# Kernel tuning notes

Hardware: AMD Instinct MI355X
Metric: run time of the kernel (lower is better)

## Reference

```python
import jax, jax.numpy as jnp
import numpy as np

BATCH = 256
B_TYPES = 32   # input capsule types
C_TYPES = 10   # output capsule types
H, W = 8, 8    # input spatial extent == kernel (output is 1x1)
POSE = 16      # capsule pose length (shape (16,1))
NUM_ITER = 3
EPS = 1e-8


def setup_inputs() -> dict:
    key = jax.random.key(0)
    k1, k2, k3 = jax.random.split(key, 3)
    input_caps_poses = jax.random.normal(k1, (BATCH, B_TYPES, H, W, POSE, 1), jnp.float32)
    input_caps_activations = jax.random.uniform(k2, (BATCH, B_TYPES, H, W), jnp.float32)
    # nn.init.normal_(std=0.1) on [B, kh, kw, C, os0, is0]
    weight = 0.1 * jax.random.normal(k3, (B_TYPES, H, W, C_TYPES, POSE, POSE), jnp.float32)
    # routing_bias initialized to 0.1: [C, oh, ow, os0, os1]
    routing_bias = jnp.full((C_TYPES, 1, 1, POSE, 1), 0.1, jnp.float32)
    return {
        "input_caps_poses": input_caps_poses,
        "input_caps_activations": input_caps_activations,
        "weight": weight,
        "routing_bias": routing_bias,
    }


def _squash(s):
    # Hinton squash: ||s||^2/(1+||s||^2) * s/||s||, norm over pose dims
    n2 = jnp.sum(s * s, axis=(-2, -1), keepdims=True)
    return (n2 / (1.0 + n2)) * s * jax.lax.rsqrt(n2 + EPS)


def reference(input_caps_poses, input_caps_activations, weight, routing_bias):
    b = input_caps_poses.shape[0]
    # votes[b,c,B,h,w,o,p] = sum_i W[B,h,w,c,o,i] * pose[b,B,h,w,i,p]
    votes = jnp.einsum('Bhwcoi,bBhwip->bcBhwop', weight, input_caps_poses)
    logits = jnp.zeros((b, C_TYPES, B_TYPES, H, W), votes.dtype)
    bias = routing_bias.reshape(1, C_TYPES, POSE, 1)
    v = None
    for it in range(NUM_ITER):
        # coupling coefficients: softmax over output capsule types
        c = jax.nn.softmax(logits, axis=1)                      # [b,C,B,h,w]
        # weighted sum of votes over all input capsules (B,h,w)
        s = jnp.einsum('bcBhw,bcBhwop->bcop', c, votes) + bias  # [b,C,16,1]
        v = _squash(s)
        if it < NUM_ITER - 1:
            # agreement: dot(vote, output pose)
            logits = logits + jnp.einsum('bcBhwop,bcop->bcBhw', votes, v)
    output_caps_poses = v[:, :, None, None, :, :]               # [b,C,1,1,16,1]
    output_caps_activations = jnp.sqrt(
        jnp.sum(v * v, axis=(-2, -1)) + EPS)[:, :, None, None]  # [b,C,1,1]
    return output_caps_poses, output_caps_activations
```

## Files before the change

kernel.cpp:

```cpp
#include <hip/hip_runtime.h>
#include <hip/hip_fp16.h>
#include <math.h>


typedef _Float16 f16;
typedef _Float16 f16x2 __attribute__((ext_vector_type(2)));
typedef _Float16 f16x4 __attribute__((ext_vector_type(4)));
typedef __fp16   h16x2 __attribute__((ext_vector_type(2)));
typedef float f32x4 __attribute__((ext_vector_type(4)));

__device__ __forceinline__ f16x2 pk(float a, float b) {
    h16x2 t = __builtin_amdgcn_cvt_pkrtz(a, b);
    return __builtin_bit_cast(f16x2, t);
}

#if __has_builtin(__builtin_amdgcn_fdot2)
__device__ __forceinline__ float FDOT2(f16x2 a, f16x2 b, float c) {
    return __builtin_amdgcn_fdot2(__builtin_bit_cast(h16x2, a),
                                  __builtin_bit_cast(h16x2, b), c, false);
}
#else
__device__ __forceinline__ float FDOT2(f16x2 a, f16x2 b, float c) {
    return c + (float)a[0] * (float)b[0] + (float)a[1] * (float)b[1];
}
#endif

constexpr int XS_ROW = 76;

__device__ __forceinline__ float xorsum4(float v) {
    v += __shfl_xor(v, 16, 64);
    v += __shfl_xor(v, 32, 64);
    return v;
}

__device__ __forceinline__ f16x2 xorsum4h(f16x2 v) {
    union { f16x2 h; int i; } u;
    union { int i; f16x2 h; } w;
    u.h = v; w.i = __shfl_xor(u.i, 16, 64); v = v + w.h;
    u.h = v; w.i = __shfl_xor(u.i, 32, 64); v = v + w.h;
    return v;
}

__device__ __forceinline__ f16x4 cvt4(float4 w) {
    f16x2 a = pk(w.x, w.y);
    f16x2 b = pk(w.z, w.w);
    f16x4 r; r[0] = a[0]; r[1] = a[1]; r[2] = b[0]; r[3] = b[1];
    return r;
}

template<int PASS>
__global__ __launch_bounds__(256, 2)
void pass_k(const float* __restrict__ poses, const float* __restrict__ weight,
            const float* __restrict__ bias,
            const float* __restrict__ sp0, const float* __restrict__ sp1,
            float* __restrict__ s_dst)
{
    __shared__ f16 Ws[640 * 16];
    __shared__ f16 xs[64 * XS_ROW];

    const int tid  = threadIdx.x;
    const int blk  = blockIdx.x;
    const int ngrp = blk >> 2;
    const int b0   = (blk & 3) * 64;
    const int wave = tid >> 6;
    const int lane = tid & 63;
    const int q    = lane >> 4;
    const int lo   = lane & 15;
    const int wtb  = wave * 16;
    const int bg   = b0 + wtb;

    const int sr  = ((lo >> 1) ^ (lo >> 3)) & 3;
    const int xqE = ((q ^ sr) & 3) * 4;
    const int xqO = ((q ^ sr ^ 2) & 3) * 4;

    f16x2 vsp[10][2];
    if (PASS >= 1) {
        const int rowb = (bg + lo) * 10;
        #pragma unroll
        for (int c = 0; c < 10; ++c) {
            float4 bb = *(const float4*)(bias + c * 16 + q * 4);
            const size_t off = (size_t)(rowb + c) * 16 + q * 4;
            float4 sa = *(const float4*)(sp0 + off);
            float t0 = sa.x + bb.x, t1 = sa.y + bb.y;
            float t2 = sa.z + bb.z, t3 = sa.w + bb.w;
            float n2 = xorsum4(t0*t0 + t1*t1 + t2*t2 + t3*t3);
            float sc = n2 / (1.f + n2) * rsqrtf(n2 + 1e-8f);
            float v0 = sc*t0, v1 = sc*t1, v2 = sc*t2, v3 = sc*t3;
            if (PASS == 2) {
                float4 ua = *(const float4*)(sp1 + off);
                float u0 = ua.x + bb.x, u1 = ua.y + bb.y;
                float u2 = ua.z + bb.z, u3 = ua.w + bb.w;
                float m2 = xorsum4(u0*u0 + u1*u1 + u2*u2 + u3*u3);
                float sc2 = m2 / (1.f + m2) * rsqrtf(m2 + 1e-8f);
                v0 += sc2*u0; v1 += sc2*u1; v2 += sc2*u2; v3 += sc2*u3;
            }
            vsp[c][0] = pk(v0, v1);
            vsp[c][1] = pk(v2, v3);
        }
    }

    f16x4 wregh[10];
    f16x4 xregh[4];
    const int b_loc = tid >> 2, part = tid & 3;
    const int wcol = (((tid & 3) ^ ((tid >> 3) ^ (tid >> 5))) & 3) * 4;

    auto load_iter = [&](int l) {
        const float* wp = weight + (size_t)(ngrp * 2 + l) * 10240;
        #pragma unroll
        for (int k = 0; k < 10; ++k) {
            float4 t = ((const float4*)wp)[tid + k * 256];
            wregh[k] = cvt4(t);
        }
        const float* xp = poses + (size_t)(b0 + b_loc) * 32768
                          + (size_t)(ngrp * 8 + l * 4 + part) * 16;
        #pragma unroll
        for (int j = 0; j < 4; ++j) {
            float4 t = ((const float4*)xp)[j];
            xregh[j] = cvt4(t);
        }
    };
    auto store_iter = [&]() {
        #pragma unroll
        for (int k = 0; k < 10; ++k) {
            const int f = tid + k * 256;
            *(f16x4*)&Ws[(f >> 2) * 16 + wcol] = wregh[k];
        }
        f16* lp = xs + b_loc * XS_ROW + part * 16;
        #pragma unroll
        for (int j = 0; j < 4; ++j) *(f16x4*)&lp[j * 4] = xregh[j];
    };

    f32x4 acc[10];
    #pragma unroll
    for (int c = 0; c < 10; ++c) acc[c] = (f32x4){0.f, 0.f, 0.f, 0.f};

    load_iter(0);

    for (int l = 0; l < 2; ++l) {
        __syncthreads();
        store_iter();
        if (l + 1 < 2) load_iter(l + 1);
        __syncthreads();

        #pragma unroll
        for (int n = 0; n < 4; ++n) {
            f16x4 bx = *(const f16x4*)&xs[(wtb + lo) * XS_ROW + n * 16 + q * 4];
            f16x2 Vh[10][2];
            #pragma unroll
            for (int c = 0; c < 10; ++c) {
                f16x4 aw = *(const f16x4*)&Ws[((n * 10 + c) * 16 + lo) * 16
                                              + ((c & 1) ? xqO : xqE)];
                f32x4 V = __builtin_amdgcn_mfma_f32_16x16x16f16(
                    aw, bx, (f32x4){0.f, 0.f, 0.f, 0.f}, 0, 0, 0);
                Vh[c][0] = pk(V[0], V[1]);
                Vh[c][1] = pk(V[2], V[3]);
            }

            float cfv[10];
            if (PASS >= 1) {
                float lg[10];
                #pragma unroll
                for (int cp = 0; cp < 5; ++cp) {
                    const int c0 = cp * 2, c1 = cp * 2 + 1;
                    float p0 = FDOT2(Vh[c0][0], vsp[c0][0], 0.f);
                    p0 = FDOT2(Vh[c0][1], vsp[c0][1], p0);
                    float p1 = FDOT2(Vh[c1][0], vsp[c1][0], 0.f);
                    p1 = FDOT2(Vh[c1][1], vsp[c1][1], p1);
                    f16x2 pr = xorsum4h(pk(p0, p1));
                    lg[c0] = (float)pr[0];
                    lg[c1] = (float)pr[1];
                }
                float m = lg[0];
                #pragma unroll
                for (int c = 1; c < 10; ++c) m = fmaxf(m, lg[c]);
                float sum = 0.f;
                #pragma unroll
                for (int c = 0; c < 10; ++c) { lg[c] = __expf(lg[c] - m); sum += lg[c]; }
                const float inv = 1.f / sum;
                #pragma unroll
                for (int c = 0; c < 10; ++c) cfv[c] = lg[c] * inv;
            }

            #pragma unroll
            for (int c = 0; c < 10; ++c) {
                const float w = (PASS == 0) ? 1.f : cfv[c];
                acc[c][0] = fmaf(w, (float)Vh[c][0][0], acc[c][0]);
                acc[c][1] = fmaf(w, (float)Vh[c][0][1], acc[c][1]);
                acc[c][2] = fmaf(w, (float)Vh[c][1][0], acc[c][2]);
                acc[c][3] = fmaf(w, (float)Vh[c][1][1], acc[c][3]);
            }
        }
    }

    __syncthreads();
    float* tr = (float*)Ws + wave * 320;
    const float fs = (PASS == 0) ? 0.1f : 1.f;
    #pragma unroll
    for (int c = 0; c < 10; ++c) {
        *(float4*)&tr[lo * 20 + q * 4] = (float4){acc[c][0], acc[c][1], acc[c][2], acc[c][3]};
        float r0 = tr[(q * 4 + 0) * 20 + lo];
        float r1 = tr[(q * 4 + 1) * 20 + lo];
        float r2 = tr[(q * 4 + 2) * 20 + lo];
        float r3 = tr[(q * 4 + 3) * 20 + lo];
        float* sp = s_dst + ((size_t)(bg + q * 4) * 10 + c) * 16 + lo;
        unsafeAtomicAdd(sp + 0 * 160, fs * r0);
        unsafeAtomicAdd(sp + 1 * 160, fs * r1);
        unsafeAtomicAdd(sp + 2 * 160, fs * r2);
        unsafeAtomicAdd(sp + 3 * 160, fs * r3);
    }
}

__global__ __launch_bounds__(256)
void epi_k(const float* __restrict__ s2, const float* __restrict__ bias,
           float* __restrict__ out)
{
    const int t = blockIdx.x * 256 + threadIdx.x;
    if (t >= 2560) return;
    const int c = t % 10;
    const float* sp = s2 + (size_t)t * 16;
    const float* bp = bias + c * 16;
    float sv[16];
    float n2 = 0.f;
    #pragma unroll
    for (int o = 0; o < 16; ++o) { float v = sp[o] + bp[o]; sv[o] = v; n2 += v * v; }
    const float scale = n2 / (1.f + n2) * rsqrtf(n2 + 1e-8f);
    float a2 = 0.f;
    #pragma unroll
    for (int o = 0; o < 16; ++o) {
        float v = scale * sv[o];
        out[(size_t)t * 16 + o] = v;
        a2 += v * v;
    }
    out[40960 + t] = sqrtf(a2 + 1e-8f);
}

extern "C" void kernel_launch(void* const* d_in, const int* in_sizes, int n_in,
                              void* d_out, int out_size, void* d_ws, size_t ws_size,
                              hipStream_t stream)
{
    const float* poses  = (const float*)d_in[0];
    const float* weight = (const float*)d_in[2];
    const float* bias   = (const float*)d_in[3];
    float* out = (float*)d_out;
    float* s0 = (float*)d_ws;
    float* s1 = s0 + 40960;
    float* s2 = s1 + 40960;

    (void)hipMemsetAsync(d_ws, 0, 3 * 40960 * sizeof(float), stream);

    pass_k<0><<<1024, 256, 0, stream>>>(poses, weight, bias, nullptr, nullptr, s0);
    pass_k<1><<<1024, 256, 0, stream>>>(poses, weight, bias, s0, nullptr, s1);
    pass_k<2><<<1024, 256, 0, stream>>>(poses, weight, bias, s0, s1, s2);
    epi_k<<<10, 256, 0, stream>>>(s2, bias, out);
}
```

Measured before the change: 247.5 us.

## Fuse routing passes into one cooperative persistent kernel with LDS-resident data

Replaces the three per-iteration routing kernels and the epilogue with a single cooperative kernel of 256 blocks × 512 threads. Each block loads its weight slice and pose tile into LDS once as fp16, then runs all three routing passes with grid.sync between them. This avoids re-reading poses and weights from global memory on every pass and removes the extra launches. The cost is a larger LDS footprint per block and fewer resident blocks, plus grid-wide barriers. The fallback to a normal launch if the cooperative launch fails would deadlock or race at grid.sync.

```diff
diff --git a/kernel.cpp b/kernel.cpp
--- a/kernel.cpp
+++ b/kernel.cpp
@@ -1,6 +1,9 @@
 #include <hip/hip_runtime.h>
 #include <hip/hip_fp16.h>
+#include <hip/hip_cooperative_groups.h>
 #include <math.h>
+
+namespace cg = cooperative_groups;
 
 
 typedef _Float16 f16;
@@ -25,7 +28,7 @@
 }
 #endif
 
-constexpr int XS_ROW = 76;
+constexpr int XS_ROW = 268;
 
 __device__ __forceinline__ float xorsum4(float v) {
     v += __shfl_xor(v, 16, 64);
@@ -48,103 +51,102 @@
     return r;
 }
 
-template<int PASS>
-__global__ __launch_bounds__(256, 2)
-void pass_k(const float* __restrict__ poses, const float* __restrict__ weight,
-            const float* __restrict__ bias,
-            const float* __restrict__ sp0, const float* __restrict__ sp1,
-            float* __restrict__ s_dst)
+__global__ __launch_bounds__(512, 2)
+void fused_k(const float* __restrict__ poses, const float* __restrict__ weight,
+             const float* __restrict__ bias,
+             float* __restrict__ s0, float* __restrict__ s1,
+             float* __restrict__ s2, float* __restrict__ out)
 {
-    __shared__ f16 Ws[640 * 16];
-    __shared__ f16 xs[64 * XS_ROW];
+    __shared__ f16   Ws[2560 * 16];
+    __shared__ f16   xs[128 * XS_ROW];
+    __shared__ float tr[8 * 320];
 
     const int tid  = threadIdx.x;
     const int blk  = blockIdx.x;
-    const int ngrp = blk >> 2;
-    const int b0   = (blk & 3) * 64;
+    const int ngrp = blk >> 1;
+    const int b0   = (blk & 1) * 128;
     const int wave = tid >> 6;
     const int lane = tid & 63;
     const int q    = lane >> 4;
     const int lo   = lane & 15;
-    const int wtb  = wave * 16;
-    const int bg   = b0 + wtb;
+    const int bg   = b0 + wave * 16;
 
     const int sr  = ((lo >> 1) ^ (lo >> 3)) & 3;
     const int xqE = ((q ^ sr) & 3) * 4;
     const int xqO = ((q ^ sr ^ 2) & 3) * 4;
 
-    f16x2 vsp[10][2];
-    if (PASS >= 1) {
-        const int rowb = (bg + lo) * 10;
-        #pragma unroll
-        for (int c = 0; c < 10; ++c) {
-            float4 bb = *(const float4*)(bias + c * 16 + q * 4);
-            const size_t off = (size_t)(rowb + c) * 16 + q * 4;
-            float4 sa = *(const float4*)(sp0 + off);
-            float t0 = sa.x + bb.x, t1 = sa.y + bb.y;
-            float t2 = sa.z + bb.z, t3 = sa.w + bb.w;
-            float n2 = xorsum4(t0*t0 + t1*t1 + t2*t2 + t3*t3);
-            float sc = n2 / (1.f + n2) * rsqrtf(n2 + 1e-8f);
-            float v0 = sc*t0, v1 = sc*t1, v2 = sc*t2, v3 = sc*t3;
-            if (PASS == 2) {
-                float4 ua = *(const float4*)(sp1 + off);
-                float u0 = ua.x + bb.x, u1 = ua.y + bb.y;
-                float u2 = ua.z + bb.z, u3 = ua.w + bb.w;
-                float m2 = xorsum4(u0*u0 + u1*u1 + u2*u2 + u3*u3);
-                float sc2 = m2 / (1.f + m2) * rsqrtf(m2 + 1e-8f);
-                v0 += sc2*u0; v1 += sc2*u1; v2 += sc2*u2; v3 += sc2*u3;
-            }
-            vsp[c][0] = pk(v0, v1);
-            vsp[c][1] = pk(v2, v3);
-        }
-    }
-
-    f16x4 wregh[10];
-    f16x4 xregh[4];
-    const int b_loc = tid >> 2, part = tid & 3;
-    const int wcol = (((tid & 3) ^ ((tid >> 3) ^ (tid >> 5))) & 3) * 4;
-
-    auto load_iter = [&](int l) {
-        const float* wp = weight + (size_t)(ngrp * 2 + l) * 10240;
-        #pragma unroll
-        for (int k = 0; k < 10; ++k) {
-            float4 t = ((const float4*)wp)[tid + k * 256];
-            wregh[k] = cvt4(t);
-        }
+    {
+        const float* wp = weight + (size_t)ngrp * 40960;
+        const int wcol = (((tid & 3) ^ ((tid >> 3) ^ (tid >> 5))) & 3) * 4;
+        float4 wreg[10];
+        #pragma unroll
+        for (int half = 0; half < 2; ++half) {
+            #pragma unroll
+            for (int k = 0; k < 10; ++k)
+                wreg[k] = ((const float4*)wp)[tid + (half * 10 + k) * 512];
+            #pragma unroll
+            for (int k = 0; k < 10; ++k) {
+                const int f = tid + (half * 10 + k) * 512;
+                *(f16x4*)&Ws[(f >> 2) * 16 + wcol] = cvt4(wreg[k]);
+            }
+        }
+        const int b_loc = tid >> 2, part = tid & 3;
         const float* xp = poses + (size_t)(b0 + b_loc) * 32768
-                          + (size_t)(ngrp * 8 + l * 4 + part) * 16;
-        #pragma unroll
-        for (int j = 0; j < 4; ++j) {
-            float4 t = ((const float4*)xp)[j];
-            xregh[j] = cvt4(t);
-        }
-    };
-    auto store_iter = [&]() {
-        #pragma unroll
-        for (int k = 0; k < 10; ++k) {
-            const int f = tid + k * 256;
-            *(f16x4*)&Ws[(f >> 2) * 16 + wcol] = wregh[k];
-        }
-        f16* lp = xs + b_loc * XS_ROW + part * 16;
-        #pragma unroll
-        for (int j = 0; j < 4; ++j) *(f16x4*)&lp[j * 4] = xregh[j];
-    };
-
-    f32x4 acc[10];
-    #pragma unroll
-    for (int c = 0; c < 10; ++c) acc[c] = (f32x4){0.f, 0.f, 0.f, 0.f};
-
-    load_iter(0);
-
-    for (int l = 0; l < 2; ++l) {
-        __syncthreads();
-        store_iter();
-        if (l + 1 < 2) load_iter(l + 1);
-        __syncthreads();
-
-        #pragma unroll
-        for (int n = 0; n < 4; ++n) {
-            f16x4 bx = *(const f16x4*)&xs[(wtb + lo) * XS_ROW + n * 16 + q * 4];
+                          + (size_t)ngrp * 256 + part * 64;
+        float4 xreg[8];
+        #pragma unroll
+        for (int half = 0; half < 2; ++half) {
+            #pragma unroll
+            for (int j = 0; j < 8; ++j)
+                xreg[j] = ((const float4*)xp)[half * 8 + j];
+            #pragma unroll
+            for (int j = 0; j < 8; ++j)
+                *(f16x4*)&xs[b_loc * XS_ROW + part * 64 + (half * 8 + j) * 4]
+                    = cvt4(xreg[j]);
+        }
+    }
+    __syncthreads();
+
+    cg::grid_group grid = cg::this_grid();
+
+    #pragma unroll 1
+    for (int pass = 0; pass < 3; ++pass) {
+        float* dst = (pass == 0) ? s0 : (pass == 1) ? s1 : s2;
+        const float fs = (pass == 0) ? 0.1f : 1.f;
+
+        f16x2 vsp[10][2];
+        if (pass >= 1) {
+            const int rowb = (bg + lo) * 10;
+            #pragma unroll
+            for (int c = 0; c < 10; ++c) {
+                float4 bb = *(const float4*)(bias + c * 16 + q * 4);
+                const size_t off = (size_t)(rowb + c) * 16 + q * 4;
+                float4 sa = *(const float4*)(s0 + off);
+                float t0 = sa.x + bb.x, t1 = sa.y + bb.y;
+                float t2 = sa.z + bb.z, t3 = sa.w + bb.w;
+                float n2 = xorsum4(t0*t0 + t1*t1 + t2*t2 + t3*t3);
+                float sc = n2 / (1.f + n2) * rsqrtf(n2 + 1e-8f);
+                float v0 = sc*t0, v1 = sc*t1, v2 = sc*t2, v3 = sc*t3;
+                if (pass == 2) {
+                    float4 ua = *(const float4*)(s1 + off);
+                    float u0 = ua.x + bb.x, u1 = ua.y + bb.y;
+                    float u2 = ua.z + bb.z, u3 = ua.w + bb.w;
+                    float m2 = xorsum4(u0*u0 + u1*u1 + u2*u2 + u3*u3);
+                    float sc2 = m2 / (1.f + m2) * rsqrtf(m2 + 1e-8f);
+                    v0 += sc2*u0; v1 += sc2*u1; v2 += sc2*u2; v3 += sc2*u3;
+                }
+                vsp[c][0] = pk(v0, v1);
+                vsp[c][1] = pk(v2, v3);
+            }
+        }
+
+        f32x4 acc[10];
+        #pragma unroll
+        for (int c = 0; c < 10; ++c) acc[c] = (f32x4){0.f, 0.f, 0.f, 0.f};
+
+        #pragma unroll 2
+        for (int n = 0; n < 16; ++n) {
+            f16x4 bx = *(const f16x4*)&xs[(wave * 16 + lo) * XS_ROW + n * 16 + q * 4];
             f16x2 Vh[10][2];
             #pragma unroll
             for (int c = 0; c < 10; ++c) {
@@ -157,7 +159,9 @@
             }
 
             float cfv[10];
-            if (PASS >= 1) {
+            #pragma unroll
+            for (int c = 0; c < 10; ++c) cfv[c] = 1.f;
+            if (pass >= 1) {
                 float lg[10];
                 #pragma unroll
                 for (int cp = 0; cp < 5; ++cp) {
@@ -183,55 +187,52 @@
 
             #pragma unroll
             for (int c = 0; c < 10; ++c) {
-                const float w = (PASS == 0) ? 1.f : cfv[c];
-                acc[c][0] = fmaf(w, (float)Vh[c][0][0], acc[c][0]);
-                acc[c][1] = fmaf(w, (float)Vh[c][0][1], acc[c][1]);
-                acc[c][2] = fmaf(w, (float)Vh[c][1][0], acc[c][2]);
-                acc[c][3] = fmaf(w, (float)Vh[c][1][1], acc[c][3]);
-            }
-        }
-    }
-
-    __syncthreads();
-    float* tr = (float*)Ws + wave * 320;
-    const float fs = (PASS == 0) ? 0.1f : 1.f;
-    #pragma unroll
-    for (int c = 0; c < 10; ++c) {
-        *(float4*)&tr[lo * 20 + q * 4] = (float4){acc[c][0], acc[c][1], acc[c][2], acc[c][3]};
-        float r0 = tr[(q * 4 + 0) * 20 + lo];
-        float r1 = tr[(q * 4 + 1) * 20 + lo];
-        float r2 = tr[(q * 4 + 2) * 20 + lo];
-        float r3 = tr[(q * 4 + 3) * 20 + lo];
-        float* sp = s_dst + ((size_t)(bg + q * 4) * 10 + c) * 16 + lo;
-        unsafeAtomicAdd(sp + 0 * 160, fs * r0);
-        unsafeAtomicAdd(sp + 1 * 160, fs * r1);
-        unsafeAtomicAdd(sp + 2 * 160, fs * r2);
-        unsafeAtomicAdd(sp + 3 * 160, fs * r3);
-    }
-}
-
-__global__ __launch_bounds__(256)
-void epi_k(const float* __restrict__ s2, const float* __restrict__ bias,
-           float* __restrict__ out)
-{
-    const int t = blockIdx.x * 256 + threadIdx.x;
-    if (t >= 2560) return;
-    const int c = t % 10;
-    const float* sp = s2 + (size_t)t * 16;
-    const float* bp = bias + c * 16;
-    float sv[16];
-    float n2 = 0.f;
-    #pragma unroll
-    for (int o = 0; o < 16; ++o) { float v = sp[o] + bp[o]; sv[o] = v; n2 += v * v; }
-    const float scale = n2 / (1.f + n2) * rsqrtf(n2 + 1e-8f);
-    float a2 = 0.f;
-    #pragma unroll
-    for (int o = 0; o < 16; ++o) {
-        float v = scale * sv[o];
-        out[(size_t)t * 16 + o] = v;
-        a2 += v * v;
-    }
-    out[40960 + t] = sqrtf(a2 + 1e-8f);
+                acc[c][0] = fmaf(cfv[c], (float)Vh[c][0][0], acc[c][0]);
+                acc[c][1] = fmaf(cfv[c], (float)Vh[c][0][1], acc[c][1]);
+                acc[c][2] = fmaf(cfv[c], (float)Vh[c][1][0], acc[c][2]);
+                acc[c][3] = fmaf(cfv[c], (float)Vh[c][1][1], acc[c][3]);
+            }
+        }
+
+        float* trw = tr + wave * 320;
+        #pragma unroll
+        for (int c = 0; c < 10; ++c) {
+            *(float4*)&trw[lo * 20 + q * 4] =
+                (float4){acc[c][0], acc[c][1], acc[c][2], acc[c][3]};
+            float r0 = trw[(q * 4 + 0) * 20 + lo];
+            float r1 = trw[(q * 4 + 1) * 20 + lo];
+            float r2 = trw[(q * 4 + 2) * 20 + lo];
+            float r3 = trw[(q * 4 + 3) * 20 + lo];
+            float* sp = dst + ((size_t)(bg + q * 4) * 10 + c) * 16 + lo;
+            unsafeAtomicAdd(sp + 0 * 160, fs * r0);
+            unsafeAtomicAdd(sp + 1 * 160, fs * r1);
+            unsafeAtomicAdd(sp + 2 * 160, fs * r2);
+            unsafeAtomicAdd(sp + 3 * 160, fs * r3);
+        }
+
+        __threadfence();
+        grid.sync();
+    }
+
+    const int t = blk * 512 + tid;
+    if (t < 2560) {
+        const int c = t % 10;
+        const float* sp = s2 + (size_t)t * 16;
+        const float* bp = bias + c * 16;
+        float sv[16];
+        float n2 = 0.f;
+        #pragma unroll
+        for (int o = 0; o < 16; ++o) { float v = sp[o] + bp[o]; sv[o] = v; n2 += v * v; }
+        const float scale = n2 / (1.f + n2) * rsqrtf(n2 + 1e-8f);
+        float a2 = 0.f;
+        #pragma unroll
+        for (int o = 0; o < 16; ++o) {
+            float v = scale * sv[o];
+            out[(size_t)t * 16 + o] = v;
+            a2 += v * v;
+        }
+        out[40960 + t] = sqrtf(a2 + 1e-8f);
+    }
 }
 
 extern "C" void kernel_launch(void* const* d_in, const int* in_sizes, int n_in,
@@ -248,8 +249,12 @@
 
     (void)hipMemsetAsync(d_ws, 0, 3 * 40960 * sizeof(float), stream);
 
-    pass_k<0><<<1024, 256, 0, stream>>>(poses, weight, bias, nullptr, nullptr, s0);
-    pass_k<1><<<1024, 256, 0, stream>>>(poses, weight, bias, s0, nullptr, s1);
-    pass_k<2><<<1024, 256, 0, stream>>>(poses, weight, bias, s0, s1, s2);
-    epi_k<<<10, 256, 0, stream>>>(s2, bias, out);
-}
+    void* args[] = {(void*)&poses, (void*)&weight, (void*)&bias,
+                    (void*)&s0, (void*)&s1, (void*)&s2, (void*)&out};
+    hipError_t err = hipLaunchCooperativeKernel((const void*)fused_k,
+                                                dim3(256), dim3(512),
+                                                args, 0, stream);
+    if (err != hipSuccess) {
+        fused_k<<<256, 512, 0, stream>>>(poses, weight, bias, s0, s1, s2, out);
+    }
+}
```

Measured after the change: 369.6 us. +49.3%, slower.

## Stream weight tiles into LDS asynchronously with double buffering; keep poses in registers

Applied to the files above, without the earlier changes.

Weights are now copied straight from global memory into a double-buffered fp32 LDS tile using global_load_lds, with the next tile issued while the current one is consumed. The fp16 conversion moves to the point of use. Pose fragments are loaded directly into registers per wave instead of being staged through LDS. The goal is to overlap weight fetch with MFMA and routing work and to remove the register round trip and the extra barriers. In exchange, LDS traffic per weight read doubles and every wave repeats the same fp32-to-fp16 conversion, and the kernel relies on the barrier to wait for the async LDS loads.

```diff
diff --git a/kernel.cpp b/kernel.cpp
--- a/kernel.cpp
+++ b/kernel.cpp
@@ -24,8 +24,6 @@
     return c + (float)a[0] * (float)b[0] + (float)a[1] * (float)b[1];
 }
 #endif
-
-constexpr int XS_ROW = 76;
 
 __device__ __forceinline__ float xorsum4(float v) {
     v += __shfl_xor(v, 16, 64);
@@ -46,6 +44,21 @@
     f16x2 b = pk(w.z, w.w);
     f16x4 r; r[0] = a[0]; r[1] = a[1]; r[2] = b[0]; r[3] = b[1];
     return r;
+}
+
+#if __has_builtin(__builtin_amdgcn_global_load_lds)
+#define HAS_GLL 1
+__device__ __forceinline__ void gll16(const float* g, float* l) {
+    __builtin_amdgcn_global_load_lds(
+        (const __attribute__((address_space(1))) void*)g,
+        (__attribute__((address_space(3))) void*)l, 16, 0, 0);
+}
+#else
+#define HAS_GLL 0
+#endif
+
+__device__ __forceinline__ int sigma_row(int row) {
+    return ((row >> 1) ^ (row >> 3)) & 3;
 }
 
 template<int PASS>
@@ -55,8 +68,7 @@
             const float* __restrict__ sp0, const float* __restrict__ sp1,
             float* __restrict__ s_dst)
 {
-    __shared__ f16 Ws[640 * 16];
-    __shared__ f16 xs[64 * XS_ROW];
+    __shared__ float Ws32[2 * 5120];
 
     const int tid  = threadIdx.x;
     const int blk  = blockIdx.x;
@@ -66,12 +78,44 @@
     const int lane = tid & 63;
     const int q    = lane >> 4;
     const int lo   = lane & 15;
-    const int wtb  = wave * 16;
-    const int bg   = b0 + wtb;
+    const int bg   = b0 + wave * 16;
 
     const int sr  = ((lo >> 1) ^ (lo >> 3)) & 3;
-    const int xqE = ((q ^ sr) & 3) * 4;
-    const int xqO = ((q ^ sr ^ 2) & 3) * 4;
+    const int qE  = (q ^ sr) & 3;
+    const int qO  = qE ^ 2;
+
+    const float* wbase = weight + (size_t)ngrp * 8 * 2560;
+    auto issue_tile = [&](int t, int buf) {
+        const float* wt = wbase + (size_t)t * 5120;
+        float* db = &Ws32[buf * 5120 + (tid & 192) * 4];
+        #pragma unroll
+        for (int k = 0; k < 5; ++k) {
+            const int f   = tid + k * 256;
+            const int row = f >> 2;
+            const int sq  = (tid & 3) ^ sigma_row(row);
+            const float* src = wt + (size_t)row * 16 + sq * 4;
+#if HAS_GLL
+            float* dst = &Ws32[buf * 5120 + (k * 256 + wave * 64) * 4];
+            gll16(src, dst);
+#else
+            float4 v = *(const float4*)src;
+            *(float4*)&Ws32[buf * 5120 + f * 4] = v;
+#endif
+        }
+        (void)db;
+    };
+
+    issue_tile(0, 0);
+    issue_tile(1, 1);
+
+    f16x4 bxh[8];
+    {
+        const float4* pp = (const float4*)poses;
+        const size_t rowb = (size_t)(bg + lo) * 8192 + q;
+        #pragma unroll
+        for (int n = 0; n < 8; ++n)
+            bxh[n] = cvt4(pp[rowb + (size_t)(ngrp * 8 + n) * 4]);
+    }
 
     f16x2 vsp[10][2];
     if (PASS >= 1) {
@@ -99,57 +143,26 @@
         }
     }
 
-    f16x4 wregh[10];
-    f16x4 xregh[4];
-    const int b_loc = tid >> 2, part = tid & 3;
-    const int wcol = (((tid & 3) ^ ((tid >> 3) ^ (tid >> 5))) & 3) * 4;
-
-    auto load_iter = [&](int l) {
-        const float* wp = weight + (size_t)(ngrp * 2 + l) * 10240;
-        #pragma unroll
-        for (int k = 0; k < 10; ++k) {
-            float4 t = ((const float4*)wp)[tid + k * 256];
-            wregh[k] = cvt4(t);
-        }
-        const float* xp = poses + (size_t)(b0 + b_loc) * 32768
-                          + (size_t)(ngrp * 8 + l * 4 + part) * 16;
-        #pragma unroll
-        for (int j = 0; j < 4; ++j) {
-            float4 t = ((const float4*)xp)[j];
-            xregh[j] = cvt4(t);
-        }
-    };
-    auto store_iter = [&]() {
-        #pragma unroll
-        for (int k = 0; k < 10; ++k) {
-            const int f = tid + k * 256;
-            *(f16x4*)&Ws[(f >> 2) * 16 + wcol] = wregh[k];
-        }
-        f16* lp = xs + b_loc * XS_ROW + part * 16;
-        #pragma unroll
-        for (int j = 0; j < 4; ++j) *(f16x4*)&lp[j * 4] = xregh[j];
-    };
-
     f32x4 acc[10];
     #pragma unroll
     for (int c = 0; c < 10; ++c) acc[c] = (f32x4){0.f, 0.f, 0.f, 0.f};
 
-    load_iter(0);
-
-    for (int l = 0; l < 2; ++l) {
-        __syncthreads();
-        store_iter();
-        if (l + 1 < 2) load_iter(l + 1);
-        __syncthreads();
-
-        #pragma unroll
-        for (int n = 0; n < 4; ++n) {
-            f16x4 bx = *(const f16x4*)&xs[(wtb + lo) * XS_ROW + n * 16 + q * 4];
+    __syncthreads();
+
+    #pragma unroll 1
+    for (int t = 0; t < 4; ++t) {
+        const float4* wsf = (const float4*)&Ws32[(t & 1) * 5120];
+
+        #pragma unroll
+        for (int nl = 0; nl < 2; ++nl) {
+            const int n = t * 2 + nl;
+            f16x4 bx = bxh[n];
             f16x2 Vh[10][2];
             #pragma unroll
             for (int c = 0; c < 10; ++c) {
-                f16x4 aw = *(const f16x4*)&Ws[((n * 10 + c) * 16 + lo) * 16
-                                              + ((c & 1) ? xqO : xqE)];
+                const int row = (nl * 10 + c) * 16 + lo;
+                float4 aw4 = wsf[row * 4 + ((c & 1) ? qO : qE)];
+                f16x4 aw = cvt4(aw4);
                 f32x4 V = __builtin_amdgcn_mfma_f32_16x16x16f16(
                     aw, bx, (f32x4){0.f, 0.f, 0.f, 0.f}, 0, 0, 0);
                 Vh[c][0] = pk(V[0], V[1]);
@@ -190,14 +203,17 @@
                 acc[c][3] = fmaf(w, (float)Vh[c][1][1], acc[c][3]);
             }
         }
-    }
-
-    __syncthreads();
-    float* tr = (float*)Ws + wave * 320;
+
+        __syncthreads();
+        if (t + 2 < 4) issue_tile(t + 2, t & 1);
+    }
+
+    float* tr = (float*)Ws32 + wave * 320;
     const float fs = (PASS == 0) ? 0.1f : 1.f;
     #pragma unroll
     for (int c = 0; c < 10; ++c) {
-        *(float4*)&tr[lo * 20 + q * 4] = (float4){acc[c][0], acc[c][1], acc[c][2], acc[c][3]};
+        *(float4*)&tr[lo * 20 + q * 4] =
+            (float4){acc[c][0], acc[c][1], acc[c][2], acc[c][3]};
         float r0 = tr[(q * 4 + 0) * 20 + lo];
         float r1 = tr[(q * 4 + 1) * 20 + lo];
         float r2 = tr[(q * 4 + 2) * 20 + lo];
```

New measurement: 263.2 us. 1.06x slower.
